# Optimization experiments

Hardware: AMD Instinct MI355X
Metric: run time of the kernel (lower is better)

The kernel has to match this reference:

```python
import jax, jax.numpy as jnp
import numpy as np

D_MODEL = 1024
D_HEAD = 64


def setup_inputs() -> dict:
    key = jax.random.key(0)
    k_x, k_q, k_k, k_v, k_o = jax.random.split(key, 5)
    scale = 1.0 / np.sqrt(D_MODEL)
    residual_stream = jax.random.normal(k_x, (4, 2048, D_MODEL), dtype=jnp.float32)
    Q = scale * jax.random.normal(k_q, (D_MODEL, D_HEAD), dtype=jnp.float32)
    K = scale * jax.random.normal(k_k, (D_MODEL, D_HEAD), dtype=jnp.float32)
    V = scale * jax.random.normal(k_v, (D_MODEL, D_HEAD), dtype=jnp.float32)
    O = scale * jax.random.normal(k_o, (D_MODEL, D_HEAD), dtype=jnp.float32)
    return {"residual_stream": residual_stream, "Q": Q, "K": K, "V": V, "O": O}


def reference(residual_stream, Q, K, V, O) -> jnp.ndarray:
    # queries/keys: [B, S, d_head]
    queries = jnp.einsum('bsd,dh->bsh', residual_stream, Q)
    keys = jnp.einsum('bsd,dh->bsh', residual_stream, K)
    # NOTE: original module applies NO 1/sqrt(d_head) scaling.
    pre_attention = jnp.einsum('bqh,bkh->bqk', queries, keys)  # [B, S, S]
    S = pre_attention.shape[-1]
    causal = jnp.tril(jnp.ones((S, S), dtype=bool))
    pre_attention = jnp.where(causal[None], pre_attention, -jnp.inf)
    attention = jax.nn.softmax(pre_attention, axis=-1)
    # x = residual @ V @ O^T : [B, S, d_model]
    x = jnp.einsum('bsd,dh,eh->bse', residual_stream, V, O)
    return jnp.einsum('bqk,bke->bqe', attention, x)
```

## Files before the change

### kernel.cpp

```cpp
#include <hip/hip_runtime.h>
#include <hip/hip_bf16.h>
#include <math.h>

#define BATCH 4
#define SEQ   2048
#define DM    1024
#define DH    64
#define NROWS (BATCH*SEQ)

typedef __hip_bfloat16 bf16;
typedef __attribute__((ext_vector_type(8))) short short8;
typedef __attribute__((ext_vector_type(8))) unsigned short ushortx8;
typedef __attribute__((ext_vector_type(4))) float floatx4;

__device__ __forceinline__ ushort f2bf(float f) {
    union { bf16 h; ushort u; } cv;
    cv.h = __float2bfloat16(f);
    return cv.u;
}
__device__ __forceinline__ float bf2f(ushort u) {
    union { unsigned int i; float f; } v; v.i = ((unsigned int)u) << 16; return v.f;
}

__global__ __launch_bounds__(256) void wprep_kernel(
    const float* __restrict__ Q, const float* __restrict__ K,
    const float* __restrict__ V, const float* __restrict__ O,
    ushort* __restrict__ WhT, ushort* __restrict__ WlT,
    ushort* __restrict__ Oh, ushort* __restrict__ Ol)
{
    int n = blockIdx.x;
    if (n < 192) {
        const float* W = (n < 64) ? Q : (n < 128) ? K : V;
        int c = n & 63;
        for (int k = threadIdx.x; k < DM; k += 256) {
            float w = W[k * DH + c];
            ushort hi = f2bf(w);
            WhT[n * DM + k] = hi;
            WlT[n * DM + k] = f2bf(w - bf2f(hi));
        }
    } else {
        int e0 = (n - 192) << 4;
        for (int idx = threadIdx.x; idx < 16 * DH; idx += 256) {
            int off = (e0 << 6) + idx;
            float w = O[off];
            ushort hi = f2bf(w);
            Oh[off] = hi;
            Ol[off] = f2bf(w - bf2f(hi));
        }
    }
}

__global__ __launch_bounds__(256) void qkv_part_kernel(
    const float* __restrict__ x, const ushort* __restrict__ WhT,
    const ushort* __restrict__ WlT, float* __restrict__ Cpart)
{
    __shared__ __align__(16) ushort Xs[2][32][34];
    __shared__ __align__(16) ushort Ws[2][192][34];
    int s0 = blockIdx.x * 32;
    int kb = blockIdx.y * 256;
    int t = threadIdx.x;
    int wave = t >> 6, lane = t & 63, m_ = lane & 15, qd = lane >> 4;
    const floatx4 z4 = {0.f, 0.f, 0.f, 0.f};
    floatx4 accq[2] = {z4, z4}, acck[2] = {z4, z4}, accv[2] = {z4, z4};
    int xr = t >> 3, xc = (t & 7) * 4;
    for (int k0 = 0; k0 < 256; k0 += 32) {
        float4 v = *(const float4*)&x[(size_t)(s0 + xr) * DM + kb + k0 + xc];
        ushort h0 = f2bf(v.x), h1 = f2bf(v.y), h2 = f2bf(v.z), h3 = f2bf(v.w);
        *(ushort4*)&Xs[0][xr][xc] = make_ushort4(h0, h1, h2, h3);
        *(ushort4*)&Xs[1][xr][xc] = make_ushort4(
            f2bf(v.x - bf2f(h0)), f2bf(v.y - bf2f(h1)),
            f2bf(v.z - bf2f(h2)), f2bf(v.w - bf2f(h3)));
        #pragma unroll
        for (int j = 0; j < 3; ++j) {
            int idx = t + j * 256, n = idx >> 2, kc = (idx & 3) * 8;
            *(uint4*)&Ws[0][n][kc] = *(const uint4*)&WhT[n * DM + kb + k0 + kc];
            *(uint4*)&Ws[1][n][kc] = *(const uint4*)&WlT[n * DM + kb + k0 + kc];
        }
        __syncthreads();
        short8 ah[2], al[2];
        #pragma unroll
        for (int mi = 0; mi < 2; ++mi) {
            ah[mi] = *(const short8*)&Xs[0][mi * 16 + m_][qd * 8];
            al[mi] = *(const short8*)&Xs[1][mi * 16 + m_][qd * 8];
        }
        int nq = wave * 16 + m_, nk = 64 + wave * 16 + m_, nv = 128 + wave * 16 + m_;
        short8 bqh = *(const short8*)&Ws[0][nq][qd * 8];
        short8 bql = *(const short8*)&Ws[1][nq][qd * 8];
        short8 bkh = *(const short8*)&Ws[0][nk][qd * 8];
        short8 bkl = *(const short8*)&Ws[1][nk][qd * 8];
        short8 bvh = *(const short8*)&Ws[0][nv][qd * 8];
        #pragma unroll
        for (int mi = 0; mi < 2; ++mi) {
            accq[mi] = __builtin_amdgcn_mfma_f32_16x16x32_bf16(ah[mi], bqh, accq[mi], 0, 0, 0);
            accq[mi] = __builtin_amdgcn_mfma_f32_16x16x32_bf16(al[mi], bqh, accq[mi], 0, 0, 0);
            accq[mi] = __builtin_amdgcn_mfma_f32_16x16x32_bf16(ah[mi], bql, accq[mi], 0, 0, 0);
            acck[mi] = __builtin_amdgcn_mfma_f32_16x16x32_bf16(ah[mi], bkh, acck[mi], 0, 0, 0);
            acck[mi] = __builtin_amdgcn_mfma_f32_16x16x32_bf16(al[mi], bkh, acck[mi], 0, 0, 0);
            acck[mi] = __builtin_amdgcn_mfma_f32_16x16x32_bf16(ah[mi], bkl, acck[mi], 0, 0, 0);
            accv[mi] = __builtin_amdgcn_mfma_f32_16x16x32_bf16(ah[mi], bvh, accv[mi], 0, 0, 0);
        }
        __syncthreads();
    }
    float* Cp = Cpart + (size_t)blockIdx.y * (NROWS * 192);
    #pragma unroll
    for (int mi = 0; mi < 2; ++mi) {
        #pragma unroll
        for (int r = 0; r < 4; ++r) {
            int row = s0 + mi * 16 + qd * 4 + r;
            float* base = Cp + (size_t)row * 192;
            base[wave * 16 + m_]       = accq[mi][r];
            base[64 + wave * 16 + m_]  = acck[mi][r];
            base[128 + wave * 16 + m_] = accv[mi][r];
        }
    }
}

__global__ __launch_bounds__(256) void qkv_reduce_kernel(
    const float* __restrict__ Cpart,
    ushort* __restrict__ qh, ushort* __restrict__ ql,
    ushort* __restrict__ kh, ushort* __restrict__ kl, ushort* __restrict__ xvP)
{
    __shared__ ushort xvs[32][72];
    const size_t SL = (size_t)NROWS * 192;
    int row0 = blockIdx.x * 32;
    int t = threadIdx.x;
    #pragma unroll
    for (int i = 0; i < 24; ++i) {
        int e = i * 256 + t;
        int r = e / 192, c = e - r * 192;
        size_t row = row0 + r;
        size_t off = row * 192 + c;
        float s = Cpart[off] + Cpart[SL + off] + Cpart[2 * SL + off] + Cpart[3 * SL + off];
        ushort hi = f2bf(s);
        if (c < 64) {
            qh[row * 64 + c] = hi; ql[row * 64 + c] = f2bf(s - bf2f(hi));
        } else if (c < 128) {
            kh[row * 64 + c - 64] = hi; kl[row * 64 + c - 64] = f2bf(s - bf2f(hi));
        } else {
            xvs[r][c - 128] = hi;
        }
    }
    __syncthreads();
    int h = t & 63, qd = t >> 6;
    ushortx8 v;
    #pragma unroll
    for (int j = 0; j < 8; ++j)
        v[j] = xvs[4 * qd + (j & 3) + ((j >> 2) << 4)][h];
    int b = row0 >> 11, c32 = (row0 & 2047) >> 5;
    *(ushortx8*)&xvP[((((size_t)b << 6) + c32) * 4 + qd) * 512 + h * 8] = v;
}

__global__ __launch_bounds__(512) void attn_kernel(
    const ushort* __restrict__ qh, const ushort* __restrict__ ql,
    const ushort* __restrict__ kh, const ushort* __restrict__ kl,
    const ushort* __restrict__ xvP,
    ushort* __restrict__ Axvh, ushort* __restrict__ Axvl)
{
    __shared__ __align__(16) ushort Qs[2][2][16][72];
    __shared__ float LO[2][2][16][68];
    __shared__ float lred[8][2][16];
    int pp = blockIdx.x & 63, b = blockIdx.x >> 6;
    int srowA = pp << 4, srowB = (127 - pp) << 4;
    int t = threadIdx.x, wave = t >> 6, lane = t & 63, m_ = lane & 15, qd = lane >> 4;
    {
        int tile = t >> 8, hl = (t >> 7) & 1, r = (t >> 3) & 15, c = (t & 7) * 8;
        const ushort* src = (hl ? ql : qh) + (size_t)((b << 11) + (tile ? srowB : srowA) + r) * 64 + c;
        *(uint4*)&Qs[tile][hl][r][c] = *(const uint4*)src;
    }
    __syncthreads();
    int nA = (pp >> 2) + 1, nB = ((127 - pp) >> 2) + 1;
    int M = nA + nB;
    const ushort* khb = kh + (((size_t)b << 11)) * 64;
    const ushort* klb = kl + (((size_t)b << 11)) * 64;
    const ushort* xvb = xvP + ((size_t)b << 17);
    const floatx4 z4 = {0.f, 0.f, 0.f, 0.f};
    floatx4 accOA[4] = {z4, z4, z4, z4};
    floatx4 accOB[4] = {z4, z4, z4, z4};
    float llA = 0.f, llB = 0.f;
    for (int it = wave; it < M; it += 8) {
        int tile = (it >= nA);
        int c = tile ? (it - nA) : it;
        int srow = tile ? srowB : srowA;
        int k0 = c << 6;
        floatx4 accS[4] = {z4, z4, z4, z4};
        #pragma unroll
        for (int kk = 0; kk < 2; ++kk) {
            short8 bqh, bql;
            if (tile == 0) {
                bqh = *(const short8*)&Qs[0][0][m_][kk * 32 + qd * 8];
                bql = *(const short8*)&Qs[0][1][m_][kk * 32 + qd * 8];
            } else {
                bqh = *(const short8*)&Qs[1][0][m_][kk * 32 + qd * 8];
                bql = *(const short8*)&Qs[1][1][m_][kk * 32 + qd * 8];
            }
            #pragma unroll
            for (int mt = 0; mt < 4; ++mt) {
                size_t koff = (size_t)(k0 + mt * 16 + m_) * 64 + kk * 32 + qd * 8;
                short8 akh = *(const short8*)&khb[koff];
                short8 akl = *(const short8*)&klb[koff];
                accS[mt] = __builtin_amdgcn_mfma_f32_16x16x32_bf16(akh, bqh, accS[mt], 0, 0, 0);
                accS[mt] = __builtin_amdgcn_mfma_f32_16x16x32_bf16(akl, bqh, accS[mt], 0, 0, 0);
                accS[mt] = __builtin_amdgcn_mfma_f32_16x16x32_bf16(akh, bql, accS[mt], 0, 0, 0);
            }
        }
        int qrow = srow + m_;
        float lsum = 0.f;
        short8 pa[2];
        #pragma unroll
        for (int h2 = 0; h2 < 2; ++h2) {
            #pragma unroll
            for (int tt = 0; tt < 2; ++tt) {
                int mt = h2 * 2 + tt;
                #pragma unroll
                for (int r = 0; r < 4; ++r) {
                    int kc = k0 + mt * 16 + qd * 4 + r;
                    float p = (kc <= qrow) ? __expf(accS[mt][r]) : 0.f;
                    lsum += p;
                    pa[h2][tt * 4 + r] = (short)f2bf(p);
                }
            }
        }
        if (tile == 0) llA += lsum; else llB += lsum;
        #pragma unroll
        for (int h2 = 0; h2 < 2; ++h2) {
            int c32 = (k0 >> 5) + h2;
            const ushort* xb = xvb + ((size_t)c32 * 4 + qd) * 512 + m_ * 8;
            short8 x0 = *(const short8*)&xb[0];
            short8 x1 = *(const short8*)&xb[128];
            short8 x2 = *(const short8*)&xb[256];
            short8 x3 = *(const short8*)&xb[384];
            if (tile == 0) {
                accOA[0] = __builtin_amdgcn_mfma_f32_16x16x32_bf16(pa[h2], x0, accOA[0], 0, 0, 0);
                accOA[1] = __builtin_amdgcn_mfma_f32_16x16x32_bf16(pa[h2], x1, accOA[1], 0, 0, 0);
                accOA[2] = __builtin_amdgcn_mfma_f32_16x16x32_bf16(pa[h2], x2, accOA[2], 0, 0, 0);
                accOA[3] = __builtin_amdgcn_mfma_f32_16x16x32_bf16(pa[h2], x3, accOA[3], 0, 0, 0);
            } else {
                accOB[0] = __builtin_amdgcn_mfma_f32_16x16x32_bf16(pa[h2], x0, accOB[0], 0, 0, 0);
                accOB[1] = __builtin_amdgcn_mfma_f32_16x16x32_bf16(pa[h2], x1, accOB[1], 0, 0, 0);
                accOB[2] = __builtin_amdgcn_mfma_f32_16x16x32_bf16(pa[h2], x2, accOB[2], 0, 0, 0);
                accOB[3] = __builtin_amdgcn_mfma_f32_16x16x32_bf16(pa[h2], x3, accOB[3], 0, 0, 0);
            }
        }
    }
    llA += __shfl_xor(llA, 16); llA += __shfl_xor(llA, 32);
    llB += __shfl_xor(llB, 16); llB += __shfl_xor(llB, 32);
    if (qd == 0) { lred[wave][0][m_] = llA; lred[wave][1][m_] = llB; }
    int part = wave >> 2, w4 = wave & 3;
    for (int w = 0; w < 4; ++w) {
        if (w4 == w) {
            #pragma unroll
            for (int hn = 0; hn < 4; ++hn)
                #pragma unroll
                for (int r = 0; r < 4; ++r) {
                    int q = qd * 4 + r, h = hn * 16 + m_;
                    if (w == 0) {
                        LO[part][0][q][h] = accOA[hn][r];
                        LO[part][1][q][h] = accOB[hn][r];
                    } else {
                        LO[part][0][q][h] += accOA[hn][r];
                        LO[part][1][q][h] += accOB[hn][r];
                    }
                }
        }
        __syncthreads();
    }
    int tile2 = t >> 8, qq = (t >> 4) & 15, h0 = (t & 15) * 4;
    int srow2 = tile2 ? srowB : srowA;
    float lt = 0.f;
    #pragma unroll
    for (int w = 0; w < 8; ++w) lt += lred[w][tile2][qq];
    float sc = 1.f / lt;
    ushort4 hv, lv;
    float v0 = (LO[0][tile2][qq][h0 + 0] + LO[1][tile2][qq][h0 + 0]) * sc;
    float v1 = (LO[0][tile2][qq][h0 + 1] + LO[1][tile2][qq][h0 + 1]) * sc;
    float v2 = (LO[0][tile2][qq][h0 + 2] + LO[1][tile2][qq][h0 + 2]) * sc;
    float v3 = (LO[0][tile2][qq][h0 + 3] + LO[1][tile2][qq][h0 + 3]) * sc;
    hv.x = f2bf(v0); lv.x = f2bf(v0 - bf2f(hv.x));
    hv.y = f2bf(v1); lv.y = f2bf(v1 - bf2f(hv.y));
    hv.z = f2bf(v2); lv.z = f2bf(v2 - bf2f(hv.z));
    hv.w = f2bf(v3); lv.w = f2bf(v3 - bf2f(hv.w));
    size_t orow = (size_t)((b << 11) + srow2 + qq) * 64 + h0;
    *(ushort4*)&Axvh[orow] = hv;
    *(ushort4*)&Axvl[orow] = lv;
}

__global__ __launch_bounds__(256) void out_kernel(
    const ushort* __restrict__ Axvh, const ushort* __restrict__ Axvl,
    const ushort* __restrict__ Oh, const ushort* __restrict__ Ol,
    float* __restrict__ out)
{
    __shared__ __align__(16) ushort As[2][64][72];
    __shared__ __align__(16) ushort Bsh[2][128][72];
    int bid = blockIdx.x;
    int r0 = (bid >> 3) << 6;
    int e0 = (bid & 7) << 7;
    int t = threadIdx.x;
    {
        int tr = t >> 2, tc = (t & 3) << 4;
        const ushort* ah = Axvh + (size_t)(r0 + tr) * DH + tc;
        const ushort* al = Axvl + (size_t)(r0 + tr) * DH + tc;
        *(uint4*)&As[0][tr][tc]     = *(const uint4*)ah;
        *(uint4*)&As[0][tr][tc + 8] = *(const uint4*)(ah + 8);
        *(uint4*)&As[1][tr][tc]     = *(const uint4*)al;
        *(uint4*)&As[1][tr][tc + 8] = *(const uint4*)(al + 8);
    }
    {
        int tr = t >> 1, tc = (t & 1) << 5;
        const ushort* bh = Oh + (size_t)(e0 + tr) * DH + tc;
        const ushort* bl = Ol + (size_t)(e0 + tr) * DH + tc;
        *(uint4*)&Bsh[0][tr][tc]      = *(const uint4*)bh;
        *(uint4*)&Bsh[0][tr][tc + 8]  = *(const uint4*)(bh + 8);
        *(uint4*)&Bsh[0][tr][tc + 16] = *(const uint4*)(bh + 16);
        *(uint4*)&Bsh[0][tr][tc + 24] = *(const uint4*)(bh + 24);
        *(uint4*)&Bsh[1][tr][tc]      = *(const uint4*)bl;
        *(uint4*)&Bsh[1][tr][tc + 8]  = *(const uint4*)(bl + 8);
        *(uint4*)&Bsh[1][tr][tc + 16] = *(const uint4*)(bl + 16);
        *(uint4*)&Bsh[1][tr][tc + 24] = *(const uint4*)(bl + 24);
    }
    __syncthreads();
    int wave = t >> 6, lane = t & 63, m_ = lane & 15, qd = lane >> 4;
    const floatx4 z4 = {0.f, 0.f, 0.f, 0.f};
    floatx4 acc[8] = {z4, z4, z4, z4, z4, z4, z4, z4};
    #pragma unroll
    for (int kk = 0; kk < 2; ++kk) {
        short8 ah = *(const short8*)&As[0][wave * 16 + m_][kk * 32 + qd * 8];
        short8 al = *(const short8*)&As[1][wave * 16 + m_][kk * 32 + qd * 8];
        #pragma unroll
        for (int ni = 0; ni < 8; ++ni) {
            short8 bh = *(const short8*)&Bsh[0][ni * 16 + m_][kk * 32 + qd * 8];
            short8 bl = *(const short8*)&Bsh[1][ni * 16 + m_][kk * 32 + qd * 8];
            acc[ni] = __builtin_amdgcn_mfma_f32_16x16x32_bf16(ah, bh, acc[ni], 0, 0, 0);
            acc[ni] = __builtin_amdgcn_mfma_f32_16x16x32_bf16(al, bh, acc[ni], 0, 0, 0);
            acc[ni] = __builtin_amdgcn_mfma_f32_16x16x32_bf16(ah, bl, acc[ni], 0, 0, 0);
        }
    }
    #pragma unroll
    for (int r = 0; r < 4; ++r) {
        int row = r0 + wave * 16 + qd * 4 + r;
        float* orow = out + (size_t)row * DM + e0;
        #pragma unroll
        for (int ni = 0; ni < 8; ++ni)
            orow[ni * 16 + m_] = acc[ni][r];
    }
}

extern "C" void kernel_launch(void* const* d_in, const int* in_sizes, int n_in,
                              void* d_out, int out_size, void* d_ws, size_t ws_size,
                              hipStream_t stream) {
    const float* x = (const float*)d_in[0];
    const float* Q = (const float*)d_in[1];
    const float* K = (const float*)d_in[2];
    const float* V = (const float*)d_in[3];
    const float* O = (const float*)d_in[4];
    float* out = (float*)d_out;

    char* ws = (char*)d_ws;
    ushort* qh   = (ushort*)(ws);
    ushort* ql   = (ushort*)(ws + (1ull  << 20));
    ushort* kh   = (ushort*)(ws + (2ull  << 20));
    ushort* kl   = (ushort*)(ws + (3ull  << 20));
    ushort* xvP  = (ushort*)(ws + (4ull  << 20));
    ushort* WhT  = (ushort*)(ws + (5ull  << 20));
    ushort* WlT  = (ushort*)(ws + (5ull  << 20) + (512ull << 10));
    ushort* Oh   = (ushort*)(ws + (6ull  << 20));
    ushort* Ol   = (ushort*)(ws + (6ull  << 20) + (128ull << 10));
    ushort* Axvh = (ushort*)(ws + (7ull  << 20));
    ushort* Axvl = (ushort*)(ws + (8ull  << 20));
    float*  Cpart = (float*)(ws + (23ull << 20));

    wprep_kernel<<<256, 256, 0, stream>>>(Q, K, V, O, WhT, WlT, Oh, Ol);
    qkv_part_kernel<<<dim3(NROWS / 32, 4), 256, 0, stream>>>(x, WhT, WlT, Cpart);
    qkv_reduce_kernel<<<NROWS / 32, 256, 0, stream>>>(Cpart, qh, ql, kh, kl, xvP);
    attn_kernel<<<64 * BATCH, 512, 0, stream>>>(qh, ql, kh, kl, xvP, Axvh, Axvl);
    out_kernel<<<(NROWS / 64) * 8, 256, 0, stream>>>(Axvh, Axvl, Oh, Ol, out);
}
```

Before: 152.7 us.

## Fuse output projection into attention kernel epilogue

The attention kernel now multiplies its normalized [32 x 64] output tile by O^T directly with split-bf16 MFMAs and writes the final fp32 output. This removes the separate out_kernel launch and the round trip of Axv hi/lo through global memory. In exchange, each of only 256 attention blocks does 8 waves x 128 output columns, with B operands loaded straight from global memory and not staged in LDS, which could lengthen the attention kernel's tail.

After: 158.8 us. +3.9%, slower.

```diff
diff --git a/kernel.cpp b/kernel.cpp
--- a/kernel.cpp
+++ b/kernel.cpp
@@ -154,11 +154,13 @@
     const ushort* __restrict__ qh, const ushort* __restrict__ ql,
     const ushort* __restrict__ kh, const ushort* __restrict__ kl,
     const ushort* __restrict__ xvP,
-    ushort* __restrict__ Axvh, ushort* __restrict__ Axvl)
+    const ushort* __restrict__ Oh, const ushort* __restrict__ Ol,
+    float* __restrict__ out)
 {
     __shared__ __align__(16) ushort Qs[2][2][16][72];
     __shared__ float LO[2][2][16][68];
     __shared__ float lred[8][2][16];
+    __shared__ float lsc[2][16];
     int pp = blockIdx.x & 63, b = blockIdx.x >> 6;
     int srowA = pp << 4, srowB = (127 - pp) << 4;
     int t = threadIdx.x, wave = t >> 6, lane = t & 63, m_ = lane & 15, qd = lane >> 4;
@@ -264,83 +266,62 @@
         }
         __syncthreads();
     }
-    int tile2 = t >> 8, qq = (t >> 4) & 15, h0 = (t & 15) * 4;
-    int srow2 = tile2 ? srowB : srowA;
-    float lt = 0.f;
-    #pragma unroll
-    for (int w = 0; w < 8; ++w) lt += lred[w][tile2][qq];
-    float sc = 1.f / lt;
-    ushort4 hv, lv;
-    float v0 = (LO[0][tile2][qq][h0 + 0] + LO[1][tile2][qq][h0 + 0]) * sc;
-    float v1 = (LO[0][tile2][qq][h0 + 1] + LO[1][tile2][qq][h0 + 1]) * sc;
-    float v2 = (LO[0][tile2][qq][h0 + 2] + LO[1][tile2][qq][h0 + 2]) * sc;
-    float v3 = (LO[0][tile2][qq][h0 + 3] + LO[1][tile2][qq][h0 + 3]) * sc;
-    hv.x = f2bf(v0); lv.x = f2bf(v0 - bf2f(hv.x));
-    hv.y = f2bf(v1); lv.y = f2bf(v1 - bf2f(hv.y));
-    hv.z = f2bf(v2); lv.z = f2bf(v2 - bf2f(hv.z));
-    hv.w = f2bf(v3); lv.w = f2bf(v3 - bf2f(hv.w));
-    size_t orow = (size_t)((b << 11) + srow2 + qq) * 64 + h0;
-    *(ushort4*)&Axvh[orow] = hv;
-    *(ushort4*)&Axvl[orow] = lv;
-}
-
-__global__ __launch_bounds__(256) void out_kernel(
-    const ushort* __restrict__ Axvh, const ushort* __restrict__ Axvl,
-    const ushort* __restrict__ Oh, const ushort* __restrict__ Ol,
-    float* __restrict__ out)
-{
-    __shared__ __align__(16) ushort As[2][64][72];
-    __shared__ __align__(16) ushort Bsh[2][128][72];
-    int bid = blockIdx.x;
-    int r0 = (bid >> 3) << 6;
-    int e0 = (bid & 7) << 7;
-    int t = threadIdx.x;
-    {
-        int tr = t >> 2, tc = (t & 3) << 4;
-        const ushort* ah = Axvh + (size_t)(r0 + tr) * DH + tc;
-        const ushort* al = Axvl + (size_t)(r0 + tr) * DH + tc;
-        *(uint4*)&As[0][tr][tc]     = *(const uint4*)ah;
-        *(uint4*)&As[0][tr][tc + 8] = *(const uint4*)(ah + 8);
-        *(uint4*)&As[1][tr][tc]     = *(const uint4*)al;
-        *(uint4*)&As[1][tr][tc + 8] = *(const uint4*)(al + 8);
-    }
-    {
-        int tr = t >> 1, tc = (t & 1) << 5;
-        const ushort* bh = Oh + (size_t)(e0 + tr) * DH + tc;
-        const ushort* bl = Ol + (size_t)(e0 + tr) * DH + tc;
-        *(uint4*)&Bsh[0][tr][tc]      = *(const uint4*)bh;
-        *(uint4*)&Bsh[0][tr][tc + 8]  = *(const uint4*)(bh + 8);
-        *(uint4*)&Bsh[0][tr][tc + 16] = *(const uint4*)(bh + 16);
-        *(uint4*)&Bsh[0][tr][tc + 24] = *(const uint4*)(bh + 24);
-        *(uint4*)&Bsh[1][tr][tc]      = *(const uint4*)bl;
-        *(uint4*)&Bsh[1][tr][tc + 8]  = *(const uint4*)(bl + 8);
-        *(uint4*)&Bsh[1][tr][tc + 16] = *(const uint4*)(bl + 16);
-        *(uint4*)&Bsh[1][tr][tc + 24] = *(const uint4*)(bl + 24);
+    if (t < 32) {
+        int tile = t >> 4, q = t & 15;
+        float lt = 0.f;
+        #pragma unroll
+        for (int w = 0; w < 8; ++w) lt += lred[w][tile][q];
+        lsc[tile][q] = 1.f / lt;
     }
     __syncthreads();
-    int wave = t >> 6, lane = t & 63, m_ = lane & 15, qd = lane >> 4;
-    const floatx4 z4 = {0.f, 0.f, 0.f, 0.f};
-    floatx4 acc[8] = {z4, z4, z4, z4, z4, z4, z4, z4};
-    #pragma unroll
-    for (int kk = 0; kk < 2; ++kk) {
-        short8 ah = *(const short8*)&As[0][wave * 16 + m_][kk * 32 + qd * 8];
-        short8 al = *(const short8*)&As[1][wave * 16 + m_][kk * 32 + qd * 8];
-        #pragma unroll
-        for (int ni = 0; ni < 8; ++ni) {
-            short8 bh = *(const short8*)&Bsh[0][ni * 16 + m_][kk * 32 + qd * 8];
-            short8 bl = *(const short8*)&Bsh[1][ni * 16 + m_][kk * 32 + qd * 8];
-            acc[ni] = __builtin_amdgcn_mfma_f32_16x16x32_bf16(ah, bh, acc[ni], 0, 0, 0);
-            acc[ni] = __builtin_amdgcn_mfma_f32_16x16x32_bf16(al, bh, acc[ni], 0, 0, 0);
-            acc[ni] = __builtin_amdgcn_mfma_f32_16x16x32_bf16(ah, bl, acc[ni], 0, 0, 0);
-        }
-    }
-    #pragma unroll
-    for (int r = 0; r < 4; ++r) {
-        int row = r0 + wave * 16 + qd * 4 + r;
-        float* orow = out + (size_t)row * DM + e0;
-        #pragma unroll
-        for (int ni = 0; ni < 8; ++ni)
-            orow[ni * 16 + m_] = acc[ni][r];
+    int e0w = wave << 7;
+    short8 Ah[2][2], Al[2][2];
+    #pragma unroll
+    for (int tile = 0; tile < 2; ++tile) {
+        float sc = lsc[tile][m_];
+        #pragma unroll
+        for (int kk = 0; kk < 2; ++kk) {
+            #pragma unroll
+            for (int j = 0; j < 8; ++j) {
+                int h = kk * 32 + qd * 8 + j;
+                float v = (LO[0][tile][m_][h] + LO[1][tile][m_][h]) * sc;
+                ushort hv = f2bf(v);
+                Ah[tile][kk][j] = (short)hv;
+                Al[tile][kk][j] = (short)f2bf(v - bf2f(hv));
+            }
+        }
+    }
+    floatx4 accE[2][8];
+    #pragma unroll
+    for (int tile = 0; tile < 2; ++tile)
+        #pragma unroll
+        for (int ni = 0; ni < 8; ++ni) accE[tile][ni] = z4;
+    #pragma unroll
+    for (int ni = 0; ni < 8; ++ni) {
+        #pragma unroll
+        for (int kk = 0; kk < 2; ++kk) {
+            size_t boff = (size_t)(e0w + ni * 16 + m_) * 64 + kk * 32 + qd * 8;
+            short8 bh = *(const short8*)&Oh[boff];
+            short8 bl = *(const short8*)&Ol[boff];
+            #pragma unroll
+            for (int tile = 0; tile < 2; ++tile) {
+                accE[tile][ni] = __builtin_amdgcn_mfma_f32_16x16x32_bf16(Ah[tile][kk], bh, accE[tile][ni], 0, 0, 0);
+                accE[tile][ni] = __builtin_amdgcn_mfma_f32_16x16x32_bf16(Al[tile][kk], bh, accE[tile][ni], 0, 0, 0);
+                accE[tile][ni] = __builtin_amdgcn_mfma_f32_16x16x32_bf16(Ah[tile][kk], bl, accE[tile][ni], 0, 0, 0);
+            }
+        }
+    }
+    float* ob = out + ((size_t)b * SEQ) * DM;
+    #pragma unroll
+    for (int tile = 0; tile < 2; ++tile) {
+        int srow = tile ? srowB : srowA;
+        #pragma unroll
+        for (int r = 0; r < 4; ++r) {
+            float* orow = ob + (size_t)(srow + qd * 4 + r) * DM + e0w;
+            #pragma unroll
+            for (int ni = 0; ni < 8; ++ni)
+                orow[ni * 16 + m_] = accE[tile][ni][r];
+        }
     }
 }
 
@@ -364,13 +345,10 @@
     ushort* WlT  = (ushort*)(ws + (5ull  << 20) + (512ull << 10));
     ushort* Oh   = (ushort*)(ws + (6ull  << 20));
     ushort* Ol   = (ushort*)(ws + (6ull  << 20) + (128ull << 10));
-    ushort* Axvh = (ushort*)(ws + (7ull  << 20));
-    ushort* Axvl = (ushort*)(ws + (8ull  << 20));
     float*  Cpart = (float*)(ws + (23ull << 20));
 
     wprep_kernel<<<256, 256, 0, stream>>>(Q, K, V, O, WhT, WlT, Oh, Ol);
     qkv_part_kernel<<<dim3(NROWS / 32, 4), 256, 0, stream>>>(x, WhT, WlT, Cpart);
     qkv_reduce_kernel<<<NROWS / 32, 256, 0, stream>>>(Cpart, qh, ql, kh, kl, xvP);
-    attn_kernel<<<64 * BATCH, 512, 0, stream>>>(qh, ql, kh, kl, xvP, Axvh, Axvl);
-    out_kernel<<<(NROWS / 64) * 8, 256, 0, stream>>>(Axvh, Axvl, Oh, Ol, out);
-}
+    attn_kernel<<<64 * BATCH, 512, 0, stream>>>(qh, ql, kh, kl, xvP, Oh, Ol, out);
+}
```
